# Optimization experiments

Hardware: AMD Instinct MI355X
Metric: run time of the kernel (lower is better)

The kernel has to match this reference:

```python
import jax, jax.numpy as jnp
import numpy as np

VNUM = 50000
OUT = 128
E = 1600000
EPS = 1e-7


def setup_inputs() -> dict:
    key = jax.random.key(0)
    k = jax.random.split(key, 8)
    sidx = jax.random.randint(k[0], (E,), 0, VNUM, dtype=jnp.int64 if jax.config.jax_enable_x64 else jnp.int32)
    tidx = jax.random.randint(k[1], (E,), 0, VNUM, dtype=sidx.dtype)
    enorm = jax.random.uniform(k[2], (E,), dtype=jnp.float32)
    # edge signs +-1 as in signed graph conv
    esgn = jnp.where(jax.random.uniform(k[3], (E,)) < 0.5, -1.0, 1.0).astype(jnp.float32)
    # vrepr initialized trunc_normal(std=0.1) (zero_init=False)
    vrepr = 0.1 * jax.random.truncated_normal(k[4], -2.0, 2.0, (VNUM, OUT), dtype=jnp.float32)
    lim = 1.0 / np.sqrt(OUT)
    loc_w = jax.random.uniform(k[5], (OUT, OUT), jnp.float32, -lim, lim)
    loc_b = jnp.zeros((OUT,), jnp.float32)
    std_w = jax.random.uniform(k[6], (OUT, OUT), jnp.float32, -lim, lim)
    std_b = jnp.zeros((OUT,), jnp.float32)
    return {"sidx": sidx, "tidx": tidx, "enorm": enorm, "esgn": esgn,
            "vrepr": vrepr, "loc_w": loc_w, "loc_b": loc_b,
            "std_w": std_w, "std_b": std_b}


def reference(sidx, tidx, enorm, esgn, vrepr, loc_w, loc_b, std_w, std_b):
    # GraphConv: edge-weighted gather + scatter-add aggregation
    msg = vrepr[sidx] * (esgn * enorm)[:, None]          # [E, OUT]
    ptr = jax.ops.segment_sum(msg, tidx, num_segments=VNUM)  # [VNUM, OUT]
    loc = ptr @ loc_w.T + loc_b                          # Normal loc
    std = jax.nn.softplus(ptr @ std_w.T + std_b) + EPS   # Normal scale
    return loc, std
```

## Files before the change

kernel.cpp:

```cpp
#include <hip/hip_runtime.h>
#include <math.h>

#define VNUM 50000
#define OUTF 128
#define NEDGE 1600000
#define EPSF 1e-7f

#define CONV_BLOCKS 6250
#define BFRAG_BLOCKS 64

#define CHUNK 2048
#define NCB 49
#define COARSE_BLOCKS 782
#define BSTRIDE 36864
#define NSUB 8
#define FINE_BLOCKS (NCB * NSUB)

typedef __attribute__((ext_vector_type(8))) short short8;
typedef __attribute__((ext_vector_type(4))) float v4f;

__device__ __forceinline__ unsigned short f2bf(float f) {
    union { float f; unsigned int u; } c; c.f = f;
    unsigned int u = c.u;
    return (unsigned short)((u + 0x7FFFu + ((u >> 16) & 1u)) >> 16);
}
__device__ __forceinline__ float bf16_lo(unsigned int p) {
    union { unsigned int u; float f; } c; c.u = p << 16; return c.f;
}
__device__ __forceinline__ float bf16_hi(unsigned int p) {
    union { unsigned int u; float f; } c; c.u = p & 0xFFFF0000u; return c.f;
}

__device__ __forceinline__ int wave_incl_scan(int v, int lane) {
#pragma unroll
    for (int off = 1; off < 64; off <<= 1) {
        const int o = __shfl_up(v, off, 64);
        if (lane >= off) v += o;
    }
    return v;
}

__global__ __launch_bounds__(256) void prep_kernel(
    const float* __restrict__ vrepr, unsigned int* __restrict__ vrepr16,
    int* __restrict__ ccursor, int* __restrict__ offs,
    const float* __restrict__ loc_w, const float* __restrict__ std_w,
    unsigned int* bfrag)
{
    const int b = blockIdx.x, tid = threadIdx.x;
    if (b < CONV_BLOCKS) {
        const size_t base = (size_t)b * 1024 + tid * 4;
        const float4 v = *reinterpret_cast<const float4*>(vrepr + base);
        uint2 o;
        o.x = (unsigned)f2bf(v.x) | ((unsigned)f2bf(v.y) << 16);
        o.y = (unsigned)f2bf(v.z) | ((unsigned)f2bf(v.w) << 16);
        *reinterpret_cast<uint2*>(vrepr16 + base / 2) = o;
    } else if (b == CONV_BLOCKS) {
        if (tid < NCB) ccursor[tid] = tid * BSTRIDE;
        if (tid == 63) offs[VNUM] = NEDGE;
    } else {
        const int p = (b - (CONV_BLOCKS + 1)) * 256 + tid;
        const int j2 = p & 3, lq = (p >> 2) & 63, ks = (p >> 8) & 3, ct = p >> 10;
        const int k = ks * 32 + (lq >> 4) * 8 + j2 * 2;
        const int n = ct * 16 + (lq & 15);
        const float* wsrc = (n >> 7) ? std_w : loc_w;
        const int c = n & 127;
        bfrag[p] = (unsigned)f2bf(wsrc[c * 128 + k]) |
                   ((unsigned)f2bf(wsrc[c * 128 + k + 1]) << 16);
    }
}

__global__ __launch_bounds__(256) void coarse_kernel(
    const int* __restrict__ sidx, const int* __restrict__ tidx,
    const float* __restrict__ enorm, const float* __restrict__ esgn,
    int* __restrict__ ccursor, uint2* __restrict__ coarse8)
{
    __shared__ uint2 lrec[CHUNK];
    __shared__ int lcnt[4][NCB];
    __shared__ int lbase[4][NCB];
    __shared__ int loffs[NCB];
    __shared__ int grun[NCB];

    const int tid = threadIdx.x, lane = tid & 63, wv = tid >> 6;
    const int base = blockIdx.x * CHUNK;
    const int n = min(CHUNK, NEDGE - base);

    for (int i = tid; i < 4 * NCB; i += 256) (&lcnt[0][0])[i] = 0;
    __syncthreads();

    uint2 rec[8];
#pragma unroll
    for (int j = 0; j < 8; ++j) {
        const int e = base + j * 256 + tid;
        if (e < NEDGE) {
            const int t = tidx[e];
            const float w = esgn[e] * enorm[e];
            rec[j].x = ((unsigned)sidx[e] << 16) | (unsigned)f2bf(w);
            rec[j].y = (unsigned)t;
            atomicAdd(&lcnt[wv][t >> 10], 1);
        }
    }
    __syncthreads();

    if (tid < 64) {
        int c0 = 0, c1 = 0, c2 = 0, c3 = 0, tot = 0;
        if (lane < NCB) {
            c0 = lcnt[0][lane]; c1 = lcnt[1][lane];
            c2 = lcnt[2][lane]; c3 = lcnt[3][lane];
            tot = c0 + c1 + c2 + c3;
        }
        const int inc = wave_incl_scan(tot, lane);
        const int ex = inc - tot;
        if (lane < NCB) {
            loffs[lane]    = ex;
            lbase[0][lane] = ex;
            lbase[1][lane] = ex + c0;
            lbase[2][lane] = ex + c0 + c1;
            lbase[3][lane] = ex + c0 + c1 + c2;
            grun[lane] = atomicAdd(&ccursor[lane], tot);
        }
    }
    __syncthreads();

#pragma unroll
    for (int j = 0; j < 8; ++j) {
        const int e = base + j * 256 + tid;
        if (e < NEDGE) {
            const int cb = (int)(rec[j].y >> 10);
            const int pos = atomicAdd(&lbase[wv][cb], 1);
            lrec[pos] = rec[j];
        }
    }
    __syncthreads();

    for (int i = tid; i < n; i += 256) {
        const uint2 r = lrec[i];
        const int cb = (int)(r.y >> 10);
        coarse8[grun[cb] + (i - loffs[cb])] = r;
    }
}

__global__ __launch_bounds__(1024) void hist_kernel(
    const uint2* __restrict__ coarse8, const int* __restrict__ ccursor,
    int* __restrict__ hcnt)
{
    __shared__ int cnt[1024];
    const int tid = threadIdx.x;
    const int bin = blockIdx.x >> 3, s = blockIdx.x & 7;
    const int bs = bin * BSTRIDE;
    const int len = ccursor[bin] - bs;
    const int qs = bs + ((len * s) >> 3);
    const int qe = bs + ((len * (s + 1)) >> 3);
    cnt[tid] = 0;
    __syncthreads();
    for (int i = qs + tid; i < qe; i += 1024)
        atomicAdd(&cnt[coarse8[i].y & 1023], 1);
    __syncthreads();
    hcnt[blockIdx.x * 1024 + tid] = cnt[tid];
}

__global__ __launch_bounds__(1024) void scatter_fine_kernel(
    const uint2* __restrict__ coarse8, const int* __restrict__ ccursor,
    const int* __restrict__ hcnt, int* __restrict__ offs,
    unsigned int* __restrict__ pairs)
{
    __shared__ int cur[1024];
    __shared__ int wsum[16];
    __shared__ int sh_s0;
    const int tid = threadIdx.x, lane = tid & 63, wv = tid >> 6;
    const int bin = blockIdx.x >> 3, s = blockIdx.x & 7;
    const int bs = bin * BSTRIDE;

    if (tid < 64) {
        const int lenl = (tid < NCB) ? (ccursor[tid] - tid * BSTRIDE) : 0;
        const int incc = wave_incl_scan(lenl, tid);
        if (tid == bin) sh_s0 = incc - lenl;
    }

    const int len = ccursor[bin] - bs;
    const int qs = bs + ((len * s) >> 3);
    const int qe = bs + ((len * (s + 1)) >> 3);

    int c[NSUB];
    int tot = 0, pre = 0;
#pragma unroll
    for (int j = 0; j < NSUB; ++j) {
        c[j] = hcnt[(bin * NSUB + j) * 1024 + tid];
        tot += c[j];
        if (j < s) pre += c[j];
    }

    const int inc = wave_incl_scan(tot, lane);
    if (lane == 63) wsum[wv] = inc;
    __syncthreads();
    if (tid == 0) {
        int run = 0;
        for (int i = 0; i < 16; ++i) { const int t = wsum[i]; wsum[i] = run; run += t; }
    }
    __syncthreads();
    const int s0 = sh_s0;
    const int ex = s0 + wsum[wv] + inc - tot;
    const int gv = (bin << 10) + tid;
    if (s == 0 && gv < VNUM) offs[gv] = ex;
    cur[tid] = ex + pre;
    __syncthreads();

    for (int i = qs + tid; i < qe; i += 1024) {
        const uint2 r = coarse8[i];
        const int pos = atomicAdd(&cur[r.y & 1023], 1);
        pairs[pos] = r.x;
    }
}

__global__ __launch_bounds__(256) void aggregate_kernel(
    const int* __restrict__ offs, const unsigned int* __restrict__ pairs,
    const unsigned int* __restrict__ vrepr16, unsigned int* __restrict__ accu)
{
    const int v = blockIdx.x * 4 + (threadIdx.x >> 6);
    const int l = threadIdx.x & 63;
    int i = offs[v];
    const int end = offs[v + 1];

    float a0 = 0.0f, a1 = 0.0f;
    for (; i + 12 <= end; i += 12) {
        unsigned p[12], r[12];
#pragma unroll
        for (int j = 0; j < 12; ++j) p[j] = pairs[i + j];
#pragma unroll
        for (int j = 0; j < 12; ++j) r[j] = vrepr16[(size_t)(p[j] >> 16) * 64 + l];
#pragma unroll
        for (int j = 0; j < 12; ++j) {
            const float w = bf16_lo(p[j]);
            a0 = fmaf(bf16_lo(r[j]), w, a0);
            a1 = fmaf(bf16_hi(r[j]), w, a1);
        }
    }
    for (; i + 4 <= end; i += 4) {
        unsigned p[4], r[4];
#pragma unroll
        for (int j = 0; j < 4; ++j) p[j] = pairs[i + j];
#pragma unroll
        for (int j = 0; j < 4; ++j) r[j] = vrepr16[(size_t)(p[j] >> 16) * 64 + l];
#pragma unroll
        for (int j = 0; j < 4; ++j) {
            const float w = bf16_lo(p[j]);
            a0 = fmaf(bf16_lo(r[j]), w, a0);
            a1 = fmaf(bf16_hi(r[j]), w, a1);
        }
    }
    for (; i < end; ++i) {
        const unsigned p = pairs[i];
        const unsigned r = vrepr16[(size_t)(p >> 16) * 64 + l];
        const float w = bf16_lo(p);
        a0 = fmaf(bf16_lo(r), w, a0); a1 = fmaf(bf16_hi(r), w, a1);
    }
    const unsigned pk = (unsigned)f2bf(a0) | ((unsigned)f2bf(a1) << 16);
    __builtin_nontemporal_store(pk, accu + (size_t)v * 128 + l);
}

__global__ __launch_bounds__(256) void gemm_mfma_kernel(
    const unsigned int* accu, const unsigned int* __restrict__ bfrag,
    const float* __restrict__ loc_b, const float* __restrict__ std_b,
    float* out)
{
    __shared__ unsigned short tile[16][136];
    const int t = threadIdx.x;
    const int row0 = blockIdx.x * 16;
    const int l = t & 63, w = t >> 6;

    short8 bfr[4][4];
#pragma unroll
    for (int ct = 0; ct < 4; ++ct)
#pragma unroll
        for (int ks = 0; ks < 4; ++ks)
            bfr[ct][ks] = *reinterpret_cast<const short8*>(
                bfrag + ((((w * 4 + ct) * 4 + ks) * 64 + l) << 2));

    {
        const uint4 av = *reinterpret_cast<const uint4*>(
            accu + (size_t)(row0 + (t >> 4)) * 128 + (t & 15) * 4);
        *reinterpret_cast<uint4*>(&tile[t >> 4][(t & 15) * 8]) = av;
    }
    __syncthreads();

    const int m = l & 15, q = l >> 4;
    v4f accv[4];
#pragma unroll
    for (int ct = 0; ct < 4; ++ct) accv[ct] = (v4f){0.0f, 0.0f, 0.0f, 0.0f};

#pragma unroll
    for (int ks = 0; ks < 4; ++ks) {
        const short8 a = *reinterpret_cast<const short8*>(&tile[m][ks * 32 + q * 8]);
#pragma unroll
        for (int ct = 0; ct < 4; ++ct)
            accv[ct] = __builtin_amdgcn_mfma_f32_16x16x32_bf16(
                a, bfr[ct][ks], accv[ct], 0, 0, 0);
    }

#pragma unroll
    for (int ct = 0; ct < 4; ++ct) {
        const int colg = (w * 4 + ct) * 16 + m;
        const int h = colg >> 7, c = colg & 127;
        const float bias = (h ? std_b : loc_b)[c];
        float* dst = out + (h ? (size_t)VNUM * OUTF : (size_t)0);
#pragma unroll
        for (int reg = 0; reg < 4; ++reg) {
            const int row = row0 + q * 4 + reg;
            float x = accv[ct][reg] + bias;
            if (h) x = fmaxf(x, 0.0f) + log1pf(expf(-fabsf(x))) + EPSF;
            dst[(size_t)row * OUTF + c] = x;
        }
    }
}

__global__ __launch_bounds__(256) void gemm_fallback_kernel(
    const unsigned int* accu,
    const float* __restrict__ loc_w, const float* __restrict__ loc_b,
    const float* __restrict__ std_w, const float* __restrict__ std_b,
    float* out)
{
    __shared__ float tile[16][OUTF];
    const int t = threadIdx.x;
    const int row0 = blockIdx.x * 16;
    {
        const uint4 av = *reinterpret_cast<const uint4*>(
            accu + (size_t)(row0 + (t >> 4)) * 128 + (t & 15) * 4);
        float* dst = &tile[t >> 4][(t & 15) * 8];
        dst[0] = bf16_lo(av.x); dst[1] = bf16_hi(av.x);
        dst[2] = bf16_lo(av.y); dst[3] = bf16_hi(av.y);
        dst[4] = bf16_lo(av.z); dst[5] = bf16_hi(av.z);
        dst[6] = bf16_lo(av.w); dst[7] = bf16_hi(av.w);
    }
    __syncthreads();
    const int is_std = t >> 7;
    const int c = t & 127;
    const float* w = (is_std ? std_w : loc_w) + (size_t)c * OUTF;
    const float bias = is_std ? std_b[c] : loc_b[c];
    float accv[16];
#pragma unroll
    for (int r = 0; r < 16; ++r) accv[r] = 0.0f;
    for (int k = 0; k < OUTF; k += 4) {
        const float4 wv = *reinterpret_cast<const float4*>(w + k);
#pragma unroll
        for (int r = 0; r < 16; ++r) {
            const float4 pv = *reinterpret_cast<const float4*>(&tile[r][k]);
            float a = accv[r];
            a = fmaf(pv.x, wv.x, a); a = fmaf(pv.y, wv.y, a);
            a = fmaf(pv.z, wv.z, a); a = fmaf(pv.w, wv.w, a);
            accv[r] = a;
        }
    }
    float* dst_base = out + (is_std ? (size_t)VNUM * OUTF : (size_t)0);
#pragma unroll
    for (int r = 0; r < 16; ++r) {
        const float x = accv[r] + bias;
        dst_base[(size_t)(row0 + r) * OUTF + c] =
            is_std ? (fmaxf(x, 0.0f) + log1pf(expf(-fabsf(x))) + EPSF) : x;
    }
}

extern "C" void kernel_launch(void* const* d_in, const int* in_sizes, int n_in,
                              void* d_out, int out_size, void* d_ws, size_t ws_size,
                              hipStream_t stream) {
    const int*   sidx  = (const int*)  d_in[0];
    const int*   tidx  = (const int*)  d_in[1];
    const float* enorm = (const float*)d_in[2];
    const float* esgn  = (const float*)d_in[3];
    const float* vrepr = (const float*)d_in[4];
    const float* loc_w = (const float*)d_in[5];
    const float* loc_b = (const float*)d_in[6];
    const float* std_w = (const float*)d_in[7];
    const float* std_b = (const float*)d_in[8];

    float* out = (float*)d_out;

    uint2* coarse8 = (uint2*)out;
    unsigned int* accu = (unsigned int*)out;

    unsigned int* sbase   = (unsigned int*)(out + (size_t)VNUM * OUTF);
    unsigned int* pairs   = sbase;
    unsigned int* vrepr16 = sbase + NEDGE;
    int* offs    = (int*)(sbase + NEDGE + (size_t)VNUM * 64);
    int* ccursor = offs + VNUM + 1;
    int* hcnt    = ccursor + NCB;

    const bool use_ws = ws_size >= 16384 * sizeof(unsigned int);
    unsigned int* bfrag = use_ws ? (unsigned int*)d_ws : nullptr;

    const int prep_blocks = CONV_BLOCKS + 1 + (use_ws ? BFRAG_BLOCKS : 0);
    prep_kernel        <<<prep_blocks, 256, 0, stream>>>(vrepr, vrepr16, ccursor,
                                                         offs, loc_w, std_w, bfrag);
    coarse_kernel      <<<COARSE_BLOCKS, 256, 0, stream>>>(sidx, tidx, enorm, esgn,
                                                           ccursor, coarse8);
    hist_kernel        <<<FINE_BLOCKS, 1024, 0, stream>>>(coarse8, ccursor, hcnt);
    scatter_fine_kernel<<<FINE_BLOCKS, 1024, 0, stream>>>(coarse8, ccursor, hcnt,
                                                          offs, pairs);
    aggregate_kernel   <<<VNUM / 4, 256, 0, stream>>>(offs, pairs, vrepr16, accu);

    if (use_ws) {
        gemm_mfma_kernel<<<VNUM / 16, 256, 0, stream>>>(accu, bfrag, loc_b, std_b, out);
    } else {
        gemm_fallback_kernel<<<VNUM / 16, 256, 0, stream>>>(accu, loc_w, loc_b,
                                                            std_w, std_b, out);
    }
}
```

Measured before the change: 231.2 us.

## Fuse histogram and fine scatter into one cooperative kernel keeping records in registers

The separate histogram and fine-scatter kernels are merged into a single cooperative kernel. Each block loads its slice of coarse records into registers once, builds the local histogram, does a grid-wide sync, then scatters from registers, so coarse8 is no longer read twice. Sub-splits per bin drop from 8 to 4 so that all 196 blocks of 1024 threads can be co-resident, and the input and coarse loads use nontemporal hints. The cost is a grid barrier, register pressure from holding 9 records per thread, and a dependence on cooperative launch succeeding.

```diff
diff --git a/kernel.cpp b/kernel.cpp
--- a/kernel.cpp
+++ b/kernel.cpp
@@ -1,5 +1,8 @@
 #include <hip/hip_runtime.h>
+#include <hip/hip_cooperative_groups.h>
 #include <math.h>
+
+namespace cg = cooperative_groups;
 
 #define VNUM 50000
 #define OUTF 128
@@ -13,8 +16,9 @@
 #define NCB 49
 #define COARSE_BLOCKS 782
 #define BSTRIDE 36864
-#define NSUB 8
+#define NSUB 4
 #define FINE_BLOCKS (NCB * NSUB)
+#define RPT 9
 
 typedef __attribute__((ext_vector_type(8))) short short8;
 typedef __attribute__((ext_vector_type(4))) float v4f;
@@ -92,9 +96,11 @@
     for (int j = 0; j < 8; ++j) {
         const int e = base + j * 256 + tid;
         if (e < NEDGE) {
-            const int t = tidx[e];
-            const float w = esgn[e] * enorm[e];
-            rec[j].x = ((unsigned)sidx[e] << 16) | (unsigned)f2bf(w);
+            const int t = __builtin_nontemporal_load(tidx + e);
+            const float w = __builtin_nontemporal_load(esgn + e) *
+                            __builtin_nontemporal_load(enorm + e);
+            rec[j].x = ((unsigned)__builtin_nontemporal_load(sidx + e) << 16) |
+                       (unsigned)f2bf(w);
             rec[j].y = (unsigned)t;
             atomicAdd(&lcnt[wv][t >> 10], 1);
         }
@@ -139,35 +145,16 @@
     }
 }
 
-__global__ __launch_bounds__(1024) void hist_kernel(
+__global__ __launch_bounds__(1024) void sort_fine_kernel(
     const uint2* __restrict__ coarse8, const int* __restrict__ ccursor,
-    int* __restrict__ hcnt)
-{
-    __shared__ int cnt[1024];
-    const int tid = threadIdx.x;
-    const int bin = blockIdx.x >> 3, s = blockIdx.x & 7;
-    const int bs = bin * BSTRIDE;
-    const int len = ccursor[bin] - bs;
-    const int qs = bs + ((len * s) >> 3);
-    const int qe = bs + ((len * (s + 1)) >> 3);
-    cnt[tid] = 0;
-    __syncthreads();
-    for (int i = qs + tid; i < qe; i += 1024)
-        atomicAdd(&cnt[coarse8[i].y & 1023], 1);
-    __syncthreads();
-    hcnt[blockIdx.x * 1024 + tid] = cnt[tid];
-}
-
-__global__ __launch_bounds__(1024) void scatter_fine_kernel(
-    const uint2* __restrict__ coarse8, const int* __restrict__ ccursor,
-    const int* __restrict__ hcnt, int* __restrict__ offs,
+    int* __restrict__ hcnt, int* __restrict__ offs,
     unsigned int* __restrict__ pairs)
 {
-    __shared__ int cur[1024];
+    __shared__ int cell[1024];
     __shared__ int wsum[16];
     __shared__ int sh_s0;
     const int tid = threadIdx.x, lane = tid & 63, wv = tid >> 6;
-    const int bin = blockIdx.x >> 3, s = blockIdx.x & 7;
+    const int bin = blockIdx.x >> 2, s = blockIdx.x & 3;
     const int bs = bin * BSTRIDE;
 
     if (tid < 64) {
@@ -177,8 +164,27 @@
     }
 
     const int len = ccursor[bin] - bs;
-    const int qs = bs + ((len * s) >> 3);
-    const int qe = bs + ((len * (s + 1)) >> 3);
+    const int qs = bs + ((len * s) >> 2);
+    const int qe = bs + ((len * (s + 1)) >> 2);
+
+    cell[tid] = 0;
+    __syncthreads();
+
+    uint2 rec[RPT];
+#pragma unroll
+    for (int j = 0; j < RPT; ++j) {
+        const int idx = qs + j * 1024 + tid;
+        if (idx < qe) {
+            const uint2 r = { __builtin_nontemporal_load(&coarse8[idx].x),
+                              __builtin_nontemporal_load(&coarse8[idx].y) };
+            rec[j] = r;
+            atomicAdd(&cell[r.y & 1023], 1);
+        }
+    }
+    __syncthreads();
+    hcnt[blockIdx.x * 1024 + tid] = cell[tid];
+
+    cg::this_grid().sync();
 
     int c[NSUB];
     int tot = 0, pre = 0;
@@ -197,17 +203,19 @@
         for (int i = 0; i < 16; ++i) { const int t = wsum[i]; wsum[i] = run; run += t; }
     }
     __syncthreads();
-    const int s0 = sh_s0;
-    const int ex = s0 + wsum[wv] + inc - tot;
+    const int ex = sh_s0 + wsum[wv] + inc - tot;
     const int gv = (bin << 10) + tid;
     if (s == 0 && gv < VNUM) offs[gv] = ex;
-    cur[tid] = ex + pre;
-    __syncthreads();
-
-    for (int i = qs + tid; i < qe; i += 1024) {
-        const uint2 r = coarse8[i];
-        const int pos = atomicAdd(&cur[r.y & 1023], 1);
-        pairs[pos] = r.x;
+    cell[tid] = ex + pre;
+    __syncthreads();
+
+#pragma unroll
+    for (int j = 0; j < RPT; ++j) {
+        const int idx = qs + j * 1024 + tid;
+        if (idx < qe) {
+            const int pos = atomicAdd(&cell[rec[j].y & 1023], 1);
+            pairs[pos] = rec[j].x;
+        }
     }
 }
 
@@ -387,14 +395,22 @@
     unsigned int* bfrag = use_ws ? (unsigned int*)d_ws : nullptr;
 
     const int prep_blocks = CONV_BLOCKS + 1 + (use_ws ? BFRAG_BLOCKS : 0);
-    prep_kernel        <<<prep_blocks, 256, 0, stream>>>(vrepr, vrepr16, ccursor,
-                                                         offs, loc_w, std_w, bfrag);
-    coarse_kernel      <<<COARSE_BLOCKS, 256, 0, stream>>>(sidx, tidx, enorm, esgn,
-                                                           ccursor, coarse8);
-    hist_kernel        <<<FINE_BLOCKS, 1024, 0, stream>>>(coarse8, ccursor, hcnt);
-    scatter_fine_kernel<<<FINE_BLOCKS, 1024, 0, stream>>>(coarse8, ccursor, hcnt,
-                                                          offs, pairs);
-    aggregate_kernel   <<<VNUM / 4, 256, 0, stream>>>(offs, pairs, vrepr16, accu);
+    prep_kernel  <<<prep_blocks, 256, 0, stream>>>(vrepr, vrepr16, ccursor,
+                                                   offs, loc_w, std_w, bfrag);
+    coarse_kernel<<<COARSE_BLOCKS, 256, 0, stream>>>(sidx, tidx, enorm, esgn,
+                                                     ccursor, coarse8);
+
+    {
+        const uint2* c8 = coarse8;
+        const int* cc = ccursor;
+        void* args[] = { (void*)&c8, (void*)&cc, (void*)&hcnt,
+                         (void*)&offs, (void*)&pairs };
+        hipLaunchCooperativeKernel((const void*)sort_fine_kernel,
+                                   dim3(FINE_BLOCKS), dim3(1024),
+                                   args, 0, stream);
+    }
+
+    aggregate_kernel<<<VNUM / 4, 256, 0, stream>>>(offs, pairs, vrepr16, accu);
 
     if (use_ws) {
         gemm_mfma_kernel<<<VNUM / 16, 256, 0, stream>>>(accu, bfrag, loc_b, std_b, out);
```

Result: slower. 267.3 us (+15.6%).
